# Optimization experiments

Measured on AMD Instinct MI355X. Metric: run time of the kernel, lower is better.

Reference implementation:

```python
import jax, jax.numpy as jnp
import numpy as np

NF, D, H, HD, NL, FF = 5, 64, 8, 8, 2, 128   # features, d_model, heads, head_dim, layers, ffn
NQ, QL, NC = 8, 3, 3                          # qubits, quantum layers, classes


def pos_encoding(S, d):
    pos = np.arange(S, dtype=np.float32)[:, None]
    div = np.exp(np.arange(0, d, 2, dtype=np.float32) * (-np.log(10000.0) / d))
    pe = np.zeros((S, d), np.float32)
    pe[:, 0::2] = np.sin(pos * div)
    pe[:, 1::2] = np.cos(pos * div)
    return jnp.asarray(pe)


def layernorm(x, g, b, eps=1e-5):
    m = x.mean(-1, keepdims=True)
    v = ((x - m) ** 2).mean(-1, keepdims=True)
    return (x - m) * jax.lax.rsqrt(v + eps) * g + b


def apply1q(psi, U, w):
    # psi: (2,)*NQ complex state; apply 2x2 gate U on wire w
    p = jnp.moveaxis(psi, w, 0)
    sh = p.shape
    p = (U @ p.reshape(2, -1)).reshape(sh)
    return jnp.moveaxis(p, 0, w)


def cnot(psi, c, t):
    p = jnp.moveaxis(psi, (c, t), (0, 1))
    sh = p.shape
    p = p.reshape(2, 2, -1)
    p = jnp.stack([p[0], p[1, ::-1]], 0).reshape(sh)  # flip target when control=1
    return jnp.moveaxis(p, (0, 1), (c, t))


def rx_mat(t):
    c, s = jnp.cos(t / 2), jnp.sin(t / 2)
    return jnp.stack([jnp.stack([c + 0j, -1j * s]), jnp.stack([-1j * s, c + 0j])]).astype(jnp.complex64)


def rot_mat(phi, th, om):
    # qml.Rot = RZ(om) RY(th) RZ(phi)
    c, s = jnp.cos(th / 2), jnp.sin(th / 2)
    return jnp.stack([
        jnp.stack([jnp.exp(-0.5j * (phi + om)) * c, -jnp.exp(0.5j * (phi - om)) * s]),
        jnp.stack([jnp.exp(-0.5j * (phi - om)) * s, jnp.exp(0.5j * (phi + om)) * c]),
    ]).astype(jnp.complex64)


def quantum_circuit(angles, weights):
    # angles: [NQ], weights: [QL, NQ, 3]. Circuit: QL x (AngleEmbedding(RX) + StronglyEntanglingLayer(range=1))
    psi = jnp.zeros((2,) * NQ, jnp.complex64).at[(0,) * NQ].set(1.0)
    for l in range(QL):
        for w in range(NQ):
            psi = apply1q(psi, rx_mat(angles[w]), w)
        for w in range(NQ):
            psi = apply1q(psi, rot_mat(weights[l, w, 0], weights[l, w, 1], weights[l, w, 2]), w)
        for w in range(NQ):
            psi = cnot(psi, w, (w + 1) % NQ)
    prob = jnp.abs(psi) ** 2
    zs = []
    for w in range(NC):  # <Z_w> = p(0_w) - p(1_w)
        marg = prob.sum(axis=tuple(i for i in range(NQ) if i != w))
        zs.append(marg[0] - marg[1])
    # von Neumann entropy of wires 0..3 (trace out wires 4..7), natural log
    mat = psi.reshape(16, 16)
    rho = mat @ mat.conj().T
    ev = jnp.clip(jnp.linalg.eigvalsh(rho), 1e-10, 1.0)
    ent = -jnp.sum(ev * jnp.log(ev))
    return jnp.stack(zs), ent


def setup_inputs() -> dict:
    key = jax.random.key(0)
    ks = jax.random.split(key, 30)
    sc = 0.02
    inp = {
        'x': jax.random.normal(ks[0], (16, 1024, NF), jnp.float32),
        'Wemb': sc * jax.random.normal(ks[1], (NF, D)), 'bemb': jnp.zeros((D,)),
        'Wq': sc * jax.random.normal(ks[2], (NL, D, D)), 'bq': jnp.zeros((NL, D)),
        'Wk': sc * jax.random.normal(ks[3], (NL, D, D)), 'bk': jnp.zeros((NL, D)),
        'Wv': sc * jax.random.normal(ks[4], (NL, D, D)), 'bv': jnp.zeros((NL, D)),
        'Wo': sc * jax.random.normal(ks[5], (NL, D, D)), 'bo': jnp.zeros((NL, D)),
        'ln1g': jnp.ones((NL, D)), 'ln1b': jnp.zeros((NL, D)),
        'ln2g': jnp.ones((NL, D)), 'ln2b': jnp.zeros((NL, D)),
        'Wf1': sc * jax.random.normal(ks[6], (NL, D, FF)), 'bf1': jnp.zeros((NL, FF)),
        'Wf2': sc * jax.random.normal(ks[7], (NL, FF, D)), 'bf2': jnp.zeros((NL, D)),
        'Wp1': sc * jax.random.normal(ks[8], (D, 32)), 'bp1': jnp.zeros((32,)),
        'Wp2': sc * jax.random.normal(ks[9], (32, NQ)), 'bp2': jnp.zeros((NQ,)),
        'qweights': jax.random.normal(ks[10], (QL, NQ, 3)),
    }
    return inp


def reference(x, Wemb, bemb, Wq, bq, Wk, bk, Wv, bv, Wo, bo, ln1g, ln1b, ln2g, ln2b,
              Wf1, bf1, Wf2, bf2, Wp1, bp1, Wp2, bp2, qweights):
    B, S, _ = x.shape
    h = x @ Wemb + bemb + pos_encoding(S, D)[None]  # aug + dropout are identity in eval
    scale = np.float32(1.0 / np.sqrt(HD))
    for l in range(NL):
        q = (h @ Wq[l] + bq[l]).reshape(B, S, H, HD).transpose(0, 2, 1, 3)
        k = (h @ Wk[l] + bk[l]).reshape(B, S, H, HD).transpose(0, 2, 1, 3)
        v = (h @ Wv[l] + bv[l]).reshape(B, S, H, HD).transpose(0, 2, 1, 3)
        att = jax.nn.softmax(jnp.einsum('bhsd,bhtd->bhst', q, k) * scale, axis=-1)
        o = jnp.einsum('bhst,bhtd->bhsd', att, v).transpose(0, 2, 1, 3).reshape(B, S, D)
        h = layernorm(h + o @ Wo[l] + bo[l], ln1g[l], ln1b[l])
        ff = jax.nn.relu(h @ Wf1[l] + bf1[l]) @ Wf2[l] + bf2[l]
        h = layernorm(h + ff, ln2g[l], ln2b[l])
    pooled = h.mean(1)
    feats = jax.nn.relu(pooled @ Wp1 + bp1) @ Wp2 + bp2
    angles = jnp.tanh(feats) * np.float32(np.pi)
    logits, ent = jax.vmap(quantum_circuit, in_axes=(0, None))(angles, qweights)
    return logits, ent
```

## Files before the change

kernel.cpp:

```cpp
#include <hip/hip_runtime.h>
#include <math.h>

#define BB 16
#define SS 1024
#define NF 5
#define DD 64
#define HH 8
#define HDIM 8
#define NLAYER 2
#define FFD 128
#define NQ 8
#define QLAY 3
#define NC 3
#define NSWEEP 5
#define BHS_TOT (BB * HH * SS)

typedef __fp16 hf2 __attribute__((ext_vector_type(2)));
typedef __fp16 h8  __attribute__((ext_vector_type(8)));
typedef float  f4x __attribute__((ext_vector_type(4)));

__device__ __forceinline__ int   f2i_(float x) { union { float f; int i; } u; u.f = x; return u.i; }
__device__ __forceinline__ float i2f_(int x)   { union { float f; int i; } u; u.i = x; return u.f; }

__device__ __forceinline__ float bperm_(int pa, float x) {
    return i2f_(__builtin_amdgcn_ds_bpermute(pa, f2i_(x)));
}

__device__ __forceinline__ float half32_(float x) {
#if defined(__has_builtin)
#if __has_builtin(__builtin_amdgcn_permlane32_swap)
    int xi = f2i_(x);
    auto r = __builtin_amdgcn_permlane32_swap(xi, xi, false, false);
    int r0 = (int)r[0], r1 = (int)r[1];
    return i2f_(r0 == xi ? r1 : r0);
#else
    return __shfl_xor(x, 32);
#endif
#else
    return __shfl_xor(x, 32);
#endif
}

template<int M> __device__ __forceinline__ float lx(float x) {
    if constexpr (M == 0) {
        return x;
    } else if constexpr (M == 1) {
        return i2f_(__builtin_amdgcn_update_dpp(0, f2i_(x), 0xB1, 0xF, 0xF, true));
    } else if constexpr (M == 2) {
        return i2f_(__builtin_amdgcn_update_dpp(0, f2i_(x), 0x4E, 0xF, 0xF, true));
    } else if constexpr (M == 3) {
        return i2f_(__builtin_amdgcn_update_dpp(0, f2i_(x), 0x1B, 0xF, 0xF, true));
    } else if constexpr (M < 32) {
        return i2f_(__builtin_amdgcn_ds_swizzle(f2i_(x), (M << 10) | 0x1F));
    } else {
        return lx<M & 31>(half32_(x));
    }
}

__global__ __launch_bounds__(64) void k_embed(const float* __restrict__ x,
                                              const float* __restrict__ Wemb,
                                              const float* __restrict__ bemb,
                                              float* __restrict__ h) {
    int bs = blockIdx.x;
    int s  = bs & (SS - 1);
    int d  = threadIdx.x;
    const float* xr = x + bs * NF;
    float acc = bemb[d];
#pragma unroll
    for (int f = 0; f < NF; ++f) acc += xr[f] * Wemb[f * DD + d];
    int i = d >> 1;
    float div = expf((float)(2 * i) * (-9.210340371976184f / 64.0f));
    float ang = (float)s * div;
    float pe = (d & 1) ? cosf(ang) : sinf(ang);
    h[bs * DD + d] = acc + pe;
}

__global__ __launch_bounds__(64) void k_qkv(const float* __restrict__ h,
                                            const float* __restrict__ Wq, const float* __restrict__ bq,
                                            const float* __restrict__ Wk, const float* __restrict__ bk,
                                            const float* __restrict__ Wv, const float* __restrict__ bv,
                                            hf2* __restrict__ qh, hf2* __restrict__ kh,
                                            hf2* __restrict__ vt, int l) {
    __shared__ float hrow[4][DD];
    int d   = threadIdx.x;
    int bs0 = blockIdx.x * 4;
#pragma unroll
    for (int r = 0; r < 4; ++r) hrow[r][d] = h[(bs0 + r) * DD + d];
    __syncthreads();
    const float* wq = Wq + l * DD * DD;
    const float* wk = Wk + l * DD * DD;
    const float* wv = Wv + l * DD * DD;
    float aq[4], ak[4], av[4];
    float bqv = bq[l * DD + d], bkv = bk[l * DD + d], bvv = bv[l * DD + d];
#pragma unroll
    for (int r = 0; r < 4; ++r) { aq[r] = bqv; ak[r] = bkv; av[r] = bvv; }
#pragma unroll 4
    for (int i = 0; i < DD; ++i) {
        float wqv = wq[i * DD + d], wkv = wk[i * DD + d], wvv = wv[i * DD + d];
#pragma unroll
        for (int r = 0; r < 4; ++r) {
            float hv = hrow[r][i];
            aq[r] += hv * wqv; ak[r] += hv * wkv; av[r] += hv * wvv;
        }
    }
    int hh = d >> 3, hd = d & 7;
    const float qs = 0.3535533906f;
    float aqp[4], akp[4];
#pragma unroll
    for (int r = 0; r < 4; ++r) { aqp[r] = __shfl_xor(aq[r], 1); akp[r] = __shfl_xor(ak[r], 1); }
    if ((hd & 1) == 0) {
#pragma unroll
        for (int r = 0; r < 4; ++r) {
            int bs = bs0 + r;
            int b = bs >> 10, s = bs & 1023;
            int bhs = ((b * HH + hh) << 10) | s;
            qh[bhs * 4 + (hd >> 1)] = __builtin_amdgcn_cvt_pkrtz(aq[r] * qs, aqp[r] * qs);
            kh[bhs * 4 + (hd >> 1)] = __builtin_amdgcn_cvt_pkrtz(ak[r], akp[r]);
        }
    }
    {
        int b = bs0 >> 10, s0 = bs0 & 1023;
        int vrow = (b * HH + hh) * 8 + hd;
        hf2* vp = vt + vrow * 512 + (s0 >> 1);
        vp[0] = __builtin_amdgcn_cvt_pkrtz(av[0], av[1]);
        vp[1] = __builtin_amdgcn_cvt_pkrtz(av[2], av[3]);
    }
}

__global__ __launch_bounds__(256) void k_attn(const float4* __restrict__ qh4,
                                              const float4* __restrict__ kh4,
                                              const float4* __restrict__ vt4,
                                              float* __restrict__ Ao) {
    __shared__ float Pbuf[4][16 * 36];
    int bh  = blockIdx.x;
    int sb  = blockIdx.y;
    int tid = threadIdx.x;
    int wv  = tid >> 6;
    int L   = tid & 63;
    int m = L & 15, quad = L >> 4;
    union U { float4 f; h8 h; };
    h8 hz = {0,0,0,0,0,0,0,0};
    h8 aQ = hz;
    if (quad == 0) { U u; u.f = qh4[(bh << 10) | (sb * 64 + wv * 16 + m)]; aQ = u.h; }
    float* Pw = Pbuf[wv];
    f4x Oacc = {0.f, 0.f, 0.f, 0.f};
    float ls0 = 0.f, ls1 = 0.f, ls2 = 0.f, ls3 = 0.f;
    int rb = quad * 4;
    for (int kc = 0; kc < 32; ++kc) {
        h8 bk0 = hz, bk1 = hz;
        if (quad == 0) {
            U u0, u1;
            u0.f = kh4[(bh << 10) | (kc * 32 + m)];
            u1.f = kh4[(bh << 10) | (kc * 32 + 16 + m)];
            bk0 = u0.h; bk1 = u1.h;
        }
        f4x S0 = {0.f,0.f,0.f,0.f}, S1 = {0.f,0.f,0.f,0.f};
        S0 = __builtin_amdgcn_mfma_f32_16x16x32_f16(aQ, bk0, S0, 0, 0, 0);
        S1 = __builtin_amdgcn_mfma_f32_16x16x32_f16(aQ, bk1, S1, 0, 0, 0);
        float p00 = __expf(S0[0]), p01 = __expf(S0[1]);
        float p02 = __expf(S0[2]), p03 = __expf(S0[3]);
        float p10 = __expf(S1[0]), p11 = __expf(S1[1]);
        float p12 = __expf(S1[2]), p13 = __expf(S1[3]);
        ls0 += p00 + p10; ls1 += p01 + p11; ls2 += p02 + p12; ls3 += p03 + p13;
        Pw[(rb+0)*36 + m]      = p00; Pw[(rb+1)*36 + m]      = p01;
        Pw[(rb+2)*36 + m]      = p02; Pw[(rb+3)*36 + m]      = p03;
        Pw[(rb+0)*36 + 16 + m] = p10; Pw[(rb+1)*36 + 16 + m] = p11;
        Pw[(rb+2)*36 + 16 + m] = p12; Pw[(rb+3)*36 + 16 + m] = p13;
        float4 pa = *(const float4*)&Pw[m * 36 + quad * 8];
        float4 pb = *(const float4*)&Pw[m * 36 + quad * 8 + 4];
        hf2 c0 = __builtin_amdgcn_cvt_pkrtz(pa.x, pa.y);
        hf2 c1 = __builtin_amdgcn_cvt_pkrtz(pa.z, pa.w);
        hf2 c2 = __builtin_amdgcn_cvt_pkrtz(pb.x, pb.y);
        hf2 c3 = __builtin_amdgcn_cvt_pkrtz(pb.z, pb.w);
        h8 aP;
        aP[0] = c0[0]; aP[1] = c0[1]; aP[2] = c1[0]; aP[3] = c1[1];
        aP[4] = c2[0]; aP[5] = c2[1]; aP[6] = c3[0]; aP[7] = c3[1];
        h8 bV = hz;
        if (m < 8) {
            U uv; uv.f = vt4[((bh * 8 + m) << 7) | (kc * 4 + quad)];
            bV = uv.h;
        }
        Oacc = __builtin_amdgcn_mfma_f32_16x16x32_f16(aP, bV, Oacc, 0, 0, 0);
    }
#pragma unroll
    for (int off = 1; off <= 8; off <<= 1) {
        ls0 += __shfl_xor(ls0, off); ls1 += __shfl_xor(ls1, off);
        ls2 += __shfl_xor(ls2, off); ls3 += __shfl_xor(ls3, off);
    }
    if (m < 8) {
        int srow = sb * 64 + wv * 16 + rb;
        int base = (((bh << 10) | srow) << 3) + m;
        Ao[base]      = Oacc[0] / ls0;
        Ao[base + 8]  = Oacc[1] / ls1;
        Ao[base + 16] = Oacc[2] / ls2;
        Ao[base + 24] = Oacc[3] / ls3;
    }
}

__global__ __launch_bounds__(128) void k_mid(const float* __restrict__ Ao,
                                             const float* __restrict__ Wo, const float* __restrict__ bo,
                                             const float* __restrict__ g1, const float* __restrict__ b1,
                                             const float* __restrict__ Wf1, const float* __restrict__ bf1,
                                             const float* __restrict__ Wf2, const float* __restrict__ bf2,
                                             const float* __restrict__ g2, const float* __restrict__ b2,
                                             float* __restrict__ h, int l) {
    __shared__ float orow[4][DD];
    __shared__ float h1s[4][DD];
    __shared__ float frow[4][FFD];
    int t    = threadIdx.x;
    int d    = t & 63;
    int half = t >> 6;
    int bs0  = blockIdx.x * 4;
    int hh = d >> 3, hd = d & 7;
    int r0 = half * 2, r1 = r0 + 1;

#pragma unroll
    for (int rr = 0; rr < 2; ++rr) {
        int r  = r0 + rr;
        int bs = bs0 + r;
        int b = bs >> 10, s = bs & 1023;
        int bhs = ((b * HH + hh) << 10) | s;
        orow[r][d] = Ao[(bhs << 3) + hd];
    }
    __syncthreads();

    {
        const float* w = Wo + l * DD * DD;
        float bias = bo[l * DD + d];
        float acc0 = bias, acc1 = bias;
#pragma unroll 4
        for (int i = 0; i < DD; ++i) {
            float wv = w[i * DD + d];
            acc0 += orow[r0][i] * wv;
            acc1 += orow[r1][i] * wv;
        }
        float gg = g1[l * DD + d], bb = b1[l * DD + d];
        float accs[2] = {acc0, acc1};
#pragma unroll
        for (int rr = 0; rr < 2; ++rr) {
            int r = r0 + rr;
            float a = accs[rr] + h[(bs0 + r) * DD + d];
            float sum = a;
            for (int off = 32; off; off >>= 1) sum += __shfl_xor(sum, off);
            float mean = sum * (1.f / 64.f);
            float dx = a - mean;
            float vs = dx * dx;
            for (int off = 32; off; off >>= 1) vs += __shfl_xor(vs, off);
            float rstd = rsqrtf(vs * (1.f / 64.f) + 1e-5f);
            h1s[r][d] = dx * rstd * gg + bb;
        }
    }
    __syncthreads();

    {
        const float* w = Wf1 + l * DD * FFD;
        float bv = bf1[l * FFD + t];
        float a0 = bv, a1 = bv, a2 = bv, a3 = bv;
#pragma unroll 4
        for (int i = 0; i < DD; ++i) {
            float wv = w[i * FFD + t];
            a0 += h1s[0][i]*wv; a1 += h1s[1][i]*wv;
            a2 += h1s[2][i]*wv; a3 += h1s[3][i]*wv;
        }
        frow[0][t] = fmaxf(a0, 0.f); frow[1][t] = fmaxf(a1, 0.f);
        frow[2][t] = fmaxf(a2, 0.f); frow[3][t] = fmaxf(a3, 0.f);
    }
    __syncthreads();

    {
        const float* w = Wf2 + l * FFD * DD;
        float bias = bf2[l * DD + d];
        float acc0 = bias, acc1 = bias;
#pragma unroll 4
        for (int i = 0; i < FFD; ++i) {
            float wv = w[i * DD + d];
            acc0 += frow[r0][i] * wv;
            acc1 += frow[r1][i] * wv;
        }
        float gg = g2[l * DD + d], bb = b2[l * DD + d];
        float accs[2] = {acc0, acc1};
#pragma unroll
        for (int rr = 0; rr < 2; ++rr) {
            int r = r0 + rr;
            float a = accs[rr] + h1s[r][d];
            float sum = a;
            for (int off = 32; off; off >>= 1) sum += __shfl_xor(sum, off);
            float mean = sum * (1.f / 64.f);
            float dx = a - mean;
            float vs = dx * dx;
            for (int off = 32; off; off >>= 1) vs += __shfl_xor(vs, off);
            float rstd = rsqrtf(vs * (1.f / 64.f) + 1e-5f);
            h[(bs0 + r) * DD + d] = dx * rstd * gg + bb;
        }
    }
}

__global__ __launch_bounds__(64) void k_pool(const float* __restrict__ h, float* __restrict__ pp) {
    int b = blockIdx.x, c = blockIdx.y, d = threadIdx.x;
    const float* hp = h + (b * SS + c * 128) * DD + d;
    float acc = 0.f;
#pragma unroll 8
    for (int s = 0; s < 128; ++s) acc += hp[s * DD];
    pp[(b * 8 + c) * DD + d] = acc;
}

__global__ __launch_bounds__(64) void k_tail(const float* __restrict__ pp,
                                             const float* __restrict__ Wp1, const float* __restrict__ bp1,
                                             const float* __restrict__ Wp2, const float* __restrict__ bp2,
                                             const float* __restrict__ qw,
                                             float* __restrict__ out) {
    __shared__ float pool_s[DD];
    __shared__ float hid[32];
    __shared__ float ang_s[NQ];
    __shared__ float ucoef[QLAY * 16][8];
    __shared__ float2 Ps2[256];
    int b = blockIdx.x; int L = threadIdx.x;
    int lb4 = L << 2;

    {
        float acc = 0.f;
#pragma unroll
        for (int c = 0; c < 8; ++c) acc += pp[(b * 8 + c) * DD + L];
        pool_s[L] = acc * (1.f / 1024.f);
    }
    __syncthreads();
    if (L < 32) {
        float a = bp1[L];
#pragma unroll 8
        for (int i = 0; i < DD; ++i) a += pool_s[i] * Wp1[i * 32 + L];
        hid[L] = fmaxf(a, 0.f);
    }
    __syncthreads();
    if (L < NQ) {
        float a = bp2[L];
#pragma unroll 8
        for (int j = 0; j < 32; ++j) a += hid[j] * Wp2[j * NQ + L];
        ang_s[L] = tanhf(a) * 3.14159265358979f;
    }
    __syncthreads();

    if (L < QLAY * 16) {
        int l = L >> 4, g8 = L & 15, w = g8 & 7;
        float u00r, u00i, u01r, u01i, u10r, u10i, u11r, u11i;
        if (g8 < 8) {
            float ha = 0.5f * ang_s[w];
            float c = __cosf(ha), s = __sinf(ha);
            u00r = c;   u00i = 0.f; u01r = 0.f; u01i = -s;
            u10r = 0.f; u10i = -s;  u11r = c;   u11i = 0.f;
        } else {
            const float* p3 = qw + (l * NQ + w) * 3;
            float phi = p3[0], th = p3[1], om = p3[2];
            float ct = __cosf(0.5f * th), st = __sinf(0.5f * th);
            float al = 0.5f * (phi + om), be = 0.5f * (phi - om);
            float ca = __cosf(al), sa = __sinf(al), cb = __cosf(be), sb = __sinf(be);
            u00r =  ct * ca; u00i = -ct * sa;
            u01r = -st * cb; u01i = -st * sb;
            u10r =  st * cb; u10i = -st * sb;
            u11r =  ct * ca; u11i =  ct * sa;
        }
        float* up = ucoef[L];
        up[0] = u00r; up[1] = u00i; up[2] = u01r; up[3] = u01i;
        up[4] = u10r; up[5] = u10i; up[6] = u11r; up[7] = u11i;
    }
    __syncthreads();

    float ar[4], ai[4];
#pragma unroll
    for (int r = 0; r < 4; ++r) { ar[r] = 0.f; ai[r] = 0.f; }
    if (L == 0) ar[0] = 1.f;

#pragma unroll 1
    for (int l = 0; l < QLAY; ++l) {
#pragma unroll 1
        for (int g8 = 0; g8 < 16; ++g8) {
            const float* up = ucoef[(l << 4) | g8];
            float u00r = up[0], u00i = up[1], u01r = up[2], u01i = up[3];
            float u10r = up[4], u10i = up[5], u11r = up[6], u11i = up[7];
            int p = 7 - (g8 & 7);
            if (p >= 6) {
#pragma unroll
                for (int pi_ = 0; pi_ < 2; ++pi_) {
                    int lo = (p == 7) ? pi_ : pi_ * 2;
                    int hi = (p == 7) ? pi_ + 2 : pi_ * 2 + 1;
                    float r0 = ar[lo], m0 = ai[lo], r1 = ar[hi], m1 = ai[hi];
                    ar[lo] = u00r*r0 - u00i*m0 + u01r*r1 - u01i*m1;
                    ai[lo] = u00r*m0 + u00i*r0 + u01r*m1 + u01i*r1;
                    ar[hi] = u10r*r0 - u10i*m0 + u11r*r1 - u11i*m1;
                    ai[hi] = u10r*m0 + u10i*r0 + u11r*m1 + u11i*r1;
                }
            } else {
                int pa  = lb4 ^ (4 << p);
                int bit = (L >> p) & 1;
                float car = bit ? u11r : u00r, cai = bit ? u11i : u00i;
                float cpr = bit ? u10r : u01r, cpi = bit ? u10i : u01i;
#pragma unroll
                for (int r = 0; r < 4; ++r) {
                    float pre = bperm_(pa, ar[r]);
                    float pim = bperm_(pa, ai[r]);
                    float nr = car*ar[r] - cai*ai[r] + cpr*pre - cpi*pim;
                    float ni = car*ai[r] + cai*ar[r] + cpr*pim + cpi*pre;
                    ar[r] = nr; ai[r] = ni;
                }
            }
        }
        { float t0=ar[2]; ar[2]=ar[3]; ar[3]=t0; t0=ai[2]; ai[2]=ai[3]; ai[3]=t0; }
        ar[1] = half32_(ar[1]); ai[1] = half32_(ai[1]);
        ar[3] = half32_(ar[3]); ai[3] = half32_(ai[3]);
#pragma unroll 1
        for (int w = 2; w <= 6; ++w) {
            int pc = 7 - w, pt = 6 - w;
            int pa = lb4 ^ (4 << pt);
            bool ctrl = (L >> pc) & 1;
#pragma unroll
            for (int r = 0; r < 4; ++r) {
                float swr = bperm_(pa, ar[r]);
                float swi = bperm_(pa, ai[r]);
                ar[r] = ctrl ? swr : ar[r];
                ai[r] = ctrl ? swi : ai[r];
            }
        }
        {
            bool ctrl = L & 1;
            float n0r = ctrl ? ar[2] : ar[0], n2r = ctrl ? ar[0] : ar[2];
            float n0i = ctrl ? ai[2] : ai[0], n2i = ctrl ? ai[0] : ai[2];
            float n1r = ctrl ? ar[3] : ar[1], n3r = ctrl ? ar[1] : ar[3];
            float n1i = ctrl ? ai[3] : ai[1], n3i = ctrl ? ai[1] : ai[3];
            ar[0]=n0r; ar[1]=n1r; ar[2]=n2r; ar[3]=n3r;
            ai[0]=n0i; ai[1]=n1i; ai[2]=n2i; ai[3]=n3i;
        }
    }

    {
        float p0 = ar[0]*ar[0]+ai[0]*ai[0];
        float p1 = ar[1]*ar[1]+ai[1]*ai[1];
        float p2 = ar[2]*ar[2]+ai[2]*ai[2];
        float p3 = ar[3]*ar[3]+ai[3]*ai[3];
        float z0 = p0 + p1 - p2 - p3;
        float z1 = p0 - p1 + p2 - p3;
        float zs = p0 + p1 + p2 + p3;
        float z2 = (L & 32) ? -zs : zs;
#pragma unroll 1
        for (int off = 1; off < 64; off <<= 1) {
            int pa = lb4 ^ (off << 2);
            z0 += bperm_(pa, z0);
            z1 += bperm_(pa, z1);
            z2 += bperm_(pa, z2);
        }
        if (L == 0) {
            out[b * NC + 0] = z0;
            out[b * NC + 1] = z1;
            out[b * NC + 2] = z2;
        }
    }

#pragma unroll
    for (int r = 0; r < 4; ++r) Ps2[(r << 6) | L] = make_float2(ar[r], ai[r]);
    __syncthreads();
    int c   = L >> 2;
    int seg = L & 3;
    float gr[4], gi[4];
#pragma unroll
    for (int j = 0; j < 4; ++j) {
        float2 t = Ps2[(seg * 4 + j) * 16 + c];
        gr[j] = t.x; gi[j] = t.y;
    }
    float alm = 0.f;
#pragma unroll
    for (int j = 0; j < 4; ++j) alm += gr[j]*gr[j] + gi[j]*gi[j];
    alm += lx<1>(alm);
    alm += lx<2>(alm);

#pragma unroll 1
    for (int sweep = 0; sweep < NSWEEP; ++sweep) {
#pragma unroll 1
        for (int m = 1; m <= 15; ++m) {
            int pa = lb4 ^ (m << 4);
            float pgr[4], pgi[4];
#pragma unroll
            for (int j = 0; j < 4; ++j) {
                pgr[j] = bperm_(pa, gr[j]);
                pgi[j] = bperm_(pa, gi[j]);
            }
            float bep = bperm_(pa, alm);
            float d = 0.f, e = 0.f;
#pragma unroll
            for (int j = 0; j < 4; ++j) {
                d += gr[j]*pgr[j] + gi[j]*pgi[j];
                e += gr[j]*pgi[j] - gi[j]*pgr[j];
            }
            d += lx<1>(d); e += lx<1>(e);
            d += lx<2>(d); e += lx<2>(e);
            float g2 = d*d + e*e;
            float cth = 1.f, sth = 0.f, cph = 1.f, sph = 0.f, gn = 0.f;
            if (g2 > 1e-26f) {
                gn = __builtin_amdgcn_sqrtf(g2);
                float ginv = __builtin_amdgcn_rcpf(gn);
                cph = d * ginv; sph = -e * ginv;
                float tau = (alm - bep) * (0.5f * ginv);
                float t = ((tau >= 0.f) ? 1.f : -1.f) *
                          __builtin_amdgcn_rcpf(fabsf(tau) + __builtin_amdgcn_sqrtf(1.f + tau*tau));
                cth = __builtin_amdgcn_rsqf(1.f + t*t);
                sth = t * cth;
            }
#pragma unroll
            for (int j = 0; j < 4; ++j) {
                float er = cph*pgr[j] - sph*pgi[j];
                float ei = cph*pgi[j] + sph*pgr[j];
                gr[j] = cth * gr[j] + sth * er;
                gi[j] = cth * gi[j] + sth * ei;
            }
            alm = cth*cth*alm + sth*sth*bep + 2.f*cth*sth*gn;
        }
    }

    float alm2 = 0.f;
#pragma unroll
    for (int j = 0; j < 4; ++j) alm2 += gr[j]*gr[j] + gi[j]*gi[j];
    alm2 += lx<1>(alm2);
    alm2 += lx<2>(alm2);

    float ev = fminf(fmaxf(alm2, 1e-10f), 1.0f);
    float term = -ev * __logf(ev);
#pragma unroll 1
    for (int off = 4; off < 64; off <<= 1) term += bperm_(lb4 ^ (off << 2), term);
    if (L == 0) out[BB * NC + b] = term;
}

extern "C" void kernel_launch(void* const* d_in, const int* in_sizes, int n_in,
                              void* d_out, int out_size, void* d_ws, size_t ws_size,
                              hipStream_t stream) {
    const float* x    = (const float*)d_in[0];
    const float* Wemb = (const float*)d_in[1];
    const float* bemb = (const float*)d_in[2];
    const float* Wq   = (const float*)d_in[3];
    const float* bq   = (const float*)d_in[4];
    const float* Wk   = (const float*)d_in[5];
    const float* bk   = (const float*)d_in[6];
    const float* Wv   = (const float*)d_in[7];
    const float* bv   = (const float*)d_in[8];
    const float* Wo   = (const float*)d_in[9];
    const float* bo   = (const float*)d_in[10];
    const float* ln1g = (const float*)d_in[11];
    const float* ln1b = (const float*)d_in[12];
    const float* ln2g = (const float*)d_in[13];
    const float* ln2b = (const float*)d_in[14];
    const float* Wf1  = (const float*)d_in[15];
    const float* bf1  = (const float*)d_in[16];
    const float* Wf2  = (const float*)d_in[17];
    const float* bf2  = (const float*)d_in[18];
    const float* Wp1  = (const float*)d_in[19];
    const float* bp1  = (const float*)d_in[20];
    const float* Wp2  = (const float*)d_in[21];
    const float* bp2  = (const float*)d_in[22];
    const float* qwts = (const float*)d_in[23];
    float* out = (float*)d_out;

    const size_t M = 1u << 20;
    float* ws   = (float*)d_ws;
    float* h    = ws;
    hf2*   qh   = (hf2*)(ws + M);
    hf2*   kh   = (hf2*)(ws + M + M / 2);
    hf2*   vt   = (hf2*)(ws + 2 * M);
    float* Ao   = ws + 2 * M + M / 2;
    float* pp   = ws + 3 * M + M / 2;

    k_embed<<<BB * SS, 64, 0, stream>>>(x, Wemb, bemb, h);
    for (int l = 0; l < NLAYER; ++l) {
        k_qkv<<<BB * SS / 4, 64, 0, stream>>>(h, Wq, bq, Wk, bk, Wv, bv, qh, kh, vt, l);
        k_attn<<<dim3(BB * HH, 16), 256, 0, stream>>>((const float4*)qh, (const float4*)kh,
                                                      (const float4*)vt, Ao);
        k_mid<<<BB * SS / 4, 128, 0, stream>>>(Ao, Wo, bo, ln1g, ln1b,
                                               Wf1, bf1, Wf2, bf2, ln2g, ln2b, h, l);
    }
    k_pool<<<dim3(BB, 8), 64, 0, stream>>>(h, pp);
    k_tail<<<BB, 64, 0, stream>>>(pp, Wp1, bp1, Wp2, bp2, qwts, out);
}
```

Baseline: 297.3 us.

## Compute transposed scores so P feeds PV MFMA directly from registers

The attention kernel now computes S^T = K·Q^T by swapping the MFMA operands and permuting which keys each lane loads. The exp'd score accumulators then already sit in the A-operand layout for the P·V MFMA. This removes the per-iteration LDS round-trip (8 stores plus 2 vector loads per lane) and the shared buffer. Row sums are reduced once at the end with two cross-quad shuffles and ds_bpermute lookups, which depend on the key permutation mapping correctly onto the MFMA layout.

```diff
diff --git a/kernel.cpp b/kernel.cpp
--- a/kernel.cpp
+++ b/kernel.cpp
@@ -131,7 +131,6 @@
                                               const float4* __restrict__ kh4,
                                               const float4* __restrict__ vt4,
                                               float* __restrict__ Ao) {
-    __shared__ float Pbuf[4][16 * 36];
     int bh  = blockIdx.x;
     int sb  = blockIdx.y;
     int tid = threadIdx.x;
@@ -140,60 +139,56 @@
     int m = L & 15, quad = L >> 4;
     union U { float4 f; h8 h; };
     h8 hz = {0,0,0,0,0,0,0,0};
-    h8 aQ = hz;
-    if (quad == 0) { U u; u.f = qh4[(bh << 10) | (sb * 64 + wv * 16 + m)]; aQ = u.h; }
-    float* Pw = Pbuf[wv];
+    h8 bQ = hz;
+    if (quad == 0) { U u; u.f = qh4[(bh << 10) | (sb * 64 + wv * 16 + m)]; bQ = u.h; }
+    int kmap = 8 * (m >> 2) + (m & 3);
+    const float4* kbase = kh4 + (bh << 10);
+    const float4* vbase = vt4 + ((bh * 8 + m) << 7);
     f4x Oacc = {0.f, 0.f, 0.f, 0.f};
-    float ls0 = 0.f, ls1 = 0.f, ls2 = 0.f, ls3 = 0.f;
-    int rb = quad * 4;
+    float ls = 0.f;
     for (int kc = 0; kc < 32; ++kc) {
-        h8 bk0 = hz, bk1 = hz;
+        h8 aK0 = hz, aK1 = hz;
         if (quad == 0) {
             U u0, u1;
-            u0.f = kh4[(bh << 10) | (kc * 32 + m)];
-            u1.f = kh4[(bh << 10) | (kc * 32 + 16 + m)];
-            bk0 = u0.h; bk1 = u1.h;
+            u0.f = kbase[kc * 32 + kmap];
+            u1.f = kbase[kc * 32 + kmap + 4];
+            aK0 = u0.h; aK1 = u1.h;
         }
         f4x S0 = {0.f,0.f,0.f,0.f}, S1 = {0.f,0.f,0.f,0.f};
-        S0 = __builtin_amdgcn_mfma_f32_16x16x32_f16(aQ, bk0, S0, 0, 0, 0);
-        S1 = __builtin_amdgcn_mfma_f32_16x16x32_f16(aQ, bk1, S1, 0, 0, 0);
-        float p00 = __expf(S0[0]), p01 = __expf(S0[1]);
-        float p02 = __expf(S0[2]), p03 = __expf(S0[3]);
-        float p10 = __expf(S1[0]), p11 = __expf(S1[1]);
-        float p12 = __expf(S1[2]), p13 = __expf(S1[3]);
-        ls0 += p00 + p10; ls1 += p01 + p11; ls2 += p02 + p12; ls3 += p03 + p13;
-        Pw[(rb+0)*36 + m]      = p00; Pw[(rb+1)*36 + m]      = p01;
-        Pw[(rb+2)*36 + m]      = p02; Pw[(rb+3)*36 + m]      = p03;
-        Pw[(rb+0)*36 + 16 + m] = p10; Pw[(rb+1)*36 + 16 + m] = p11;
-        Pw[(rb+2)*36 + 16 + m] = p12; Pw[(rb+3)*36 + 16 + m] = p13;
-        float4 pa = *(const float4*)&Pw[m * 36 + quad * 8];
-        float4 pb = *(const float4*)&Pw[m * 36 + quad * 8 + 4];
-        hf2 c0 = __builtin_amdgcn_cvt_pkrtz(pa.x, pa.y);
-        hf2 c1 = __builtin_amdgcn_cvt_pkrtz(pa.z, pa.w);
-        hf2 c2 = __builtin_amdgcn_cvt_pkrtz(pb.x, pb.y);
-        hf2 c3 = __builtin_amdgcn_cvt_pkrtz(pb.z, pb.w);
+        S0 = __builtin_amdgcn_mfma_f32_16x16x32_f16(aK0, bQ, S0, 0, 0, 0);
+        S1 = __builtin_amdgcn_mfma_f32_16x16x32_f16(aK1, bQ, S1, 0, 0, 0);
+        float p0 = __expf(S0[0]), p1 = __expf(S0[1]);
+        float p2 = __expf(S0[2]), p3 = __expf(S0[3]);
+        float p4 = __expf(S1[0]), p5 = __expf(S1[1]);
+        float p6 = __expf(S1[2]), p7 = __expf(S1[3]);
+        ls += (p0 + p1 + p2 + p3) + (p4 + p5 + p6 + p7);
+        hf2 c0 = __builtin_amdgcn_cvt_pkrtz(p0, p1);
+        hf2 c1 = __builtin_amdgcn_cvt_pkrtz(p2, p3);
+        hf2 c2 = __builtin_amdgcn_cvt_pkrtz(p4, p5);
+        hf2 c3 = __builtin_amdgcn_cvt_pkrtz(p6, p7);
         h8 aP;
         aP[0] = c0[0]; aP[1] = c0[1]; aP[2] = c1[0]; aP[3] = c1[1];
         aP[4] = c2[0]; aP[5] = c2[1]; aP[6] = c3[0]; aP[7] = c3[1];
         h8 bV = hz;
         if (m < 8) {
-            U uv; uv.f = vt4[((bh * 8 + m) << 7) | (kc * 4 + quad)];
+            U uv; uv.f = vbase[kc * 4 + quad];
             bV = uv.h;
         }
         Oacc = __builtin_amdgcn_mfma_f32_16x16x32_f16(aP, bV, Oacc, 0, 0, 0);
     }
-#pragma unroll
-    for (int off = 1; off <= 8; off <<= 1) {
-        ls0 += __shfl_xor(ls0, off); ls1 += __shfl_xor(ls1, off);
-        ls2 += __shfl_xor(ls2, off); ls3 += __shfl_xor(ls3, off);
-    }
+    ls += __shfl_xor(ls, 16);
+    ls += __shfl_xor(ls, 32);
+    float d0 = bperm_((4 * quad + 0) << 2, ls);
+    float d1 = bperm_((4 * quad + 1) << 2, ls);
+    float d2 = bperm_((4 * quad + 2) << 2, ls);
+    float d3 = bperm_((4 * quad + 3) << 2, ls);
     if (m < 8) {
-        int srow = sb * 64 + wv * 16 + rb;
+        int srow = sb * 64 + wv * 16 + quad * 4;
         int base = (((bh << 10) | srow) << 3) + m;
-        Ao[base]      = Oacc[0] / ls0;
-        Ao[base + 8]  = Oacc[1] / ls1;
-        Ao[base + 16] = Oacc[2] / ls2;
-        Ao[base + 24] = Oacc[3] / ls3;
+        Ao[base]      = Oacc[0] / d0;
+        Ao[base + 8]  = Oacc[1] / d1;
+        Ao[base + 16] = Oacc[2] / d2;
+        Ao[base + 24] = Oacc[3] / d3;
     }
 }
 
```

Result: no change. 298.0 us (+0.2%).
